# Kernel tuning notes

Measured on AMD Instinct MI355X. Metric: run time of the kernel, lower is better.

Reference implementation:

```python
import jax, jax.numpy as jnp
import numpy as np


def gcn_conv(x, W, b, src, dst):
    """PyG-style GCNConv: add self-loops, symmetric normalization, then scatter-add."""
    n = x.shape[0]
    loop = jnp.arange(n, dtype=src.dtype)
    s = jnp.concatenate([src, loop])  # [E+N]
    d = jnp.concatenate([dst, loop])
    deg = jax.ops.segment_sum(jnp.ones(s.shape[0], dtype=x.dtype), d, num_segments=n)
    dinv = jax.lax.rsqrt(jnp.maximum(deg, 1.0))  # deg >= 1 due to self-loops
    norm = dinv[s] * dinv[d]                     # [E+N]
    h = x @ W                                    # [N, out]
    msg = h[s] * norm[:, None]                   # gather + scale
    return jax.ops.segment_sum(msg, d, num_segments=n) + b


def setup_inputs() -> dict:
    key = jax.random.key(0)
    ks = jax.random.split(key, 8)
    N, E, IN, H, C = 50000, 800000, 128, 64, 16
    x = jax.random.normal(ks[0], (N, IN), dtype=jnp.float32)
    edge_index = jax.random.randint(ks[1], (2, E), 0, N, dtype=jnp.int32)
    def glorot(k, shp):
        fan_in, fan_out = shp
        lim = (6.0 / (fan_in + fan_out)) ** 0.5
        return jax.random.uniform(k, shp, jnp.float32, -lim, lim)
    return {
        "x": x,
        "edge_index": edge_index,
        "W1": glorot(ks[2], (IN, H)), "b1": jnp.zeros((H,), jnp.float32),
        "W2": glorot(ks[3], (H, H)),  "b2": jnp.zeros((H,), jnp.float32),
        "Wm1": glorot(ks[4], (2 * H, H)), "bm1": jnp.zeros((H,), jnp.float32),
        "Wm2": glorot(ks[5], (H, C)),     "bm2": jnp.zeros((C,), jnp.float32),
    }


def reference(x, edge_index, W1, b1, W2, b2, Wm1, bm1, Wm2, bm2):
    src, dst = edge_index[0], edge_index[1]
    h = jax.nn.relu(gcn_conv(x, W1, b1, src, dst))
    # dropout is identity in eval mode
    h = jax.nn.relu(gcn_conv(h, W2, b2, src, dst))
    ef = jnp.concatenate([h[src], h[dst]], axis=1)  # [E, 2H]
    z = jax.nn.relu(ef @ Wm1 + bm1)
    return z @ Wm2 + bm2  # [E, numClasses]
```

## Files before the change

### kernel.cpp

```cpp
#include <hip/hip_runtime.h>
#include <hip/hip_bf16.h>

__global__ __launch_bounds__(256) void k_deg(const int* __restrict__ dst, int* __restrict__ deg, int E) {
    int e = blockIdx.x * 256 + threadIdx.x;
    if (e < E) atomicAdd(&deg[dst[e]], 1);
}

__global__ __launch_bounds__(256) void k_dinv(const int* __restrict__ deg, float* __restrict__ dinv, int N) {
    int n = blockIdx.x * 256 + threadIdx.x;
    if (n < N) dinv[n] = rsqrtf((float)(deg[n] + 1));
}

__global__ __launch_bounds__(256) void k_scan_sum(const int* __restrict__ deg, int* __restrict__ bsum, int N) {
    int n = blockIdx.x * 256 + threadIdx.x;
    int v = (n < N) ? deg[n] : 0;
#pragma unroll
    for (int o = 32; o > 0; o >>= 1) v += __shfl_down(v, o, 64);
    __shared__ int sh[4];
    if ((threadIdx.x & 63) == 0) sh[threadIdx.x >> 6] = v;
    __syncthreads();
    if (threadIdx.x == 0) bsum[blockIdx.x] = sh[0] + sh[1] + sh[2] + sh[3];
}

__global__ __launch_bounds__(256) void k_scan_off(int* __restrict__ bsum, int nb) {
    __shared__ int sh[256];
    int t = threadIdx.x;
    sh[t] = (t < nb) ? bsum[t] : 0;
    __syncthreads();
    for (int o = 1; o < 256; o <<= 1) {
        int y = (t >= o) ? sh[t - o] : 0;
        __syncthreads();
        sh[t] += y;
        __syncthreads();
    }
    if (t < nb) bsum[t] = (t == 0) ? 0 : sh[t - 1];
}

__global__ __launch_bounds__(256) void k_scan_write(const int* __restrict__ deg, const int* __restrict__ boff,
                                                    int* __restrict__ row_start, int* __restrict__ cursor, int N) {
    int n = blockIdx.x * 256 + threadIdx.x;
    int t = threadIdx.x, lane = t & 63, w = t >> 6;
    int v = (n < N) ? deg[n] : 0;
    int x = v;
#pragma unroll
    for (int o = 1; o < 64; o <<= 1) {
        int y = __shfl_up(x, o, 64);
        if (lane >= o) x += y;
    }
    __shared__ int wsum[4];
    if (lane == 63) wsum[w] = x;
    __syncthreads();
    int wo = 0;
#pragma unroll
    for (int i = 0; i < 4; ++i) wo += (i < w) ? wsum[i] : 0;
    int excl = boff[blockIdx.x] + wo + x - v;
    if (n < N) { row_start[n] = excl; cursor[n] = excl; }
    if (n == N - 1) row_start[N] = excl + v;
}

template <bool PAIR>
__global__ __launch_bounds__(256) void k_fill(const int* __restrict__ src, const int* __restrict__ dst,
                                              int* __restrict__ cursor, void* __restrict__ item, int E) {
    int e = blockIdx.x * 256 + threadIdx.x;
    if (e < E) {
        int d = dst[e];
        int pos = atomicAdd(&cursor[d], 1);
        if (PAIR) ((int2*)item)[pos] = make_int2(src[e], e);
        else      ((int*)item)[pos] = e;
    }
}

__global__ __launch_bounds__(256) void k_dvec(const int* __restrict__ rowst, int* __restrict__ dvec, int N) {
    int w = threadIdx.x >> 6, lane = threadIdx.x & 63;
    int d = blockIdx.x * 4 + w;
    if (d >= N) return;
    int beg = rowst[d], end = rowst[d + 1];
    for (int k = beg + lane; k < end; k += 64) dvec[k] = d;
}

__global__ __launch_bounds__(256) void k_tr(const float* __restrict__ in, float* __restrict__ outp, int R, int C) {
    int i = blockIdx.x * 256 + threadIdx.x;
    if (i < R * C) {
        int r = i / C, c = i % C;
        outp[(size_t)c * R + r] = in[(size_t)r * C + c];
    }
}

__global__ __launch_bounds__(256) void k_wpq(const float* __restrict__ Wm1, float* __restrict__ WPQ) {
    int i = blockIdx.x * 256 + threadIdx.x;
    if (i < 128 * 64) {
        int j = i >> 6, k = i & 63;
        WPQ[i] = (j < 64) ? Wm1[k * 64 + j] : Wm1[(64 + k) * 64 + (j - 64)];
    }
}

template <int K, bool RELU, bool BIAS, bool SCALE>
__global__ __launch_bounds__(256) void k_mm_slice(const float* __restrict__ X,
                                                  const float* __restrict__ WT,
                                                  const float* __restrict__ bias,
                                                  const float* __restrict__ dinv,
                                                  float* __restrict__ Y, int N) {
    int n = blockIdx.x * 256 + threadIdx.x;
    int j0 = blockIdx.y * 16;
    int nc = n < N ? n : N - 1;
    const float* xr = X + (size_t)nc * K;
    const float* wr = WT + (size_t)j0 * K;
    float acc[16];
#pragma unroll
    for (int j = 0; j < 16; ++j) acc[j] = BIAS ? bias[j0 + j] : 0.f;
#pragma unroll 1
    for (int k0 = 0; k0 < K; k0 += 8) {
        float ef[8];
        *(float4*)(ef)     = *(const float4*)(xr + k0);
        *(float4*)(ef + 4) = *(const float4*)(xr + k0 + 4);
        if (RELU) {
#pragma unroll
            for (int kk = 0; kk < 8; ++kk) ef[kk] = fmaxf(ef[kk], 0.f);
        }
#pragma unroll
        for (int j = 0; j < 16; ++j) {
#pragma unroll
            for (int kk = 0; kk < 8; ++kk)
                acc[j] = fmaf(ef[kk], wr[j * K + k0 + kk], acc[j]);
        }
    }
    if (n < N) {
        if (SCALE) {
            float dn = dinv[n];
#pragma unroll
            for (int j = 0; j < 16; ++j) acc[j] *= dn;
        }
        float4* yp = (float4*)(Y + (size_t)n * 64 + j0);
#pragma unroll
        for (int q = 0; q < 4; ++q) yp[q] = *(float4*)(acc + q * 4);
    }
}

__global__ __launch_bounds__(256) void k_pq_slice(const float* __restrict__ A2,
                                                  const float* __restrict__ WPQ,
                                                  const float* __restrict__ bm1,
                                                  float* __restrict__ Pb, float* __restrict__ Qb, int N) {
    int n = blockIdx.x * 256 + threadIdx.x;
    int j0g = blockIdx.y * 16;
    bool isP = j0g < 64;
    int jo = isP ? j0g : j0g - 64;
    float* Y = isP ? Pb : Qb;
    int nc = n < N ? n : N - 1;
    const float* xr = A2 + (size_t)nc * 64;
    const float* wr = WPQ + (size_t)j0g * 64;
    float acc[16];
#pragma unroll
    for (int j = 0; j < 16; ++j) acc[j] = isP ? bm1[jo + j] : 0.f;
#pragma unroll 1
    for (int k0 = 0; k0 < 64; k0 += 8) {
        float ef[8];
        *(float4*)(ef)     = *(const float4*)(xr + k0);
        *(float4*)(ef + 4) = *(const float4*)(xr + k0 + 4);
#pragma unroll
        for (int kk = 0; kk < 8; ++kk) ef[kk] = fmaxf(ef[kk], 0.f);
#pragma unroll
        for (int j = 0; j < 16; ++j)
#pragma unroll
            for (int kk = 0; kk < 8; ++kk)
                acc[j] = fmaf(ef[kk], wr[j * 64 + k0 + kk], acc[j]);
    }
    if (n < N) {
        float4* yp = (float4*)(Y + (size_t)n * 64 + jo);
#pragma unroll
        for (int q = 0; q < 4; ++q) yp[q] = *(float4*)(acc + q * 4);
    }
}

template <bool PAIR>
__global__ __launch_bounds__(256) void k_gather(const float* __restrict__ hs, const float* __restrict__ dinv,
                                                const int* __restrict__ row_start, const void* __restrict__ item,
                                                const int* __restrict__ srcArr,
                                                const float* __restrict__ bias,
                                                float* __restrict__ a, int N) {
    int w = threadIdx.x >> 6, lane = threadIdx.x & 63;
    int d = blockIdx.x * 4 + w;
    if (d >= N) return;
    int beg = row_start[d], end = row_start[d + 1];
    float dd = dinv[d];
    float acc = hs[(size_t)d * 64 + lane];
    int k = beg;
    for (; k + 8 <= end; k += 8) {
        int ss[8];
        if (PAIR) {
            const int2* it = (const int2*)item;
#pragma unroll
            for (int u = 0; u < 8; ++u) ss[u] = it[k + u].x;
        } else {
            const int* eid = (const int*)item;
            int ee[8];
#pragma unroll
            for (int u = 0; u < 8; ++u) ee[u] = eid[k + u];
#pragma unroll
            for (int u = 0; u < 8; ++u) ss[u] = srcArr[ee[u]];
        }
        float v[8];
#pragma unroll
        for (int u = 0; u < 8; ++u) v[u] = hs[(size_t)ss[u] * 64 + lane];
#pragma unroll
        for (int u = 0; u < 8; ++u) acc += v[u];
    }
    for (; k < end; ++k) {
        int s = PAIR ? ((const int2*)item)[k].x : srcArr[((const int*)item)[k]];
        acc += hs[(size_t)s * 64 + lane];
    }
    a[(size_t)d * 64 + lane] = fmaf(acc, dd, bias[lane]);
}

__global__ __launch_bounds__(256) void k_p_inplace(float* __restrict__ A2P,
                                                   const float* __restrict__ WPQ,
                                                   const float* __restrict__ bm1, int N) {
    int n = blockIdx.x * 256 + threadIdx.x;
    int nc = n < N ? n : N - 1;
    const float* xr = A2P + (size_t)nc * 64;
    float acc[64];
#pragma unroll
    for (int j = 0; j < 64; ++j) acc[j] = bm1[j];
#pragma unroll 1
    for (int k0 = 0; k0 < 64; k0 += 8) {
        float ef[8];
        *(float4*)(ef)     = *(const float4*)(xr + k0);
        *(float4*)(ef + 4) = *(const float4*)(xr + k0 + 4);
#pragma unroll
        for (int kk = 0; kk < 8; ++kk) ef[kk] = fmaxf(ef[kk], 0.f);
#pragma unroll
        for (int j = 0; j < 64; ++j)
#pragma unroll
            for (int kk = 0; kk < 8; ++kk)
                acc[j] = fmaf(ef[kk], WPQ[j * 64 + k0 + kk], acc[j]);
    }
    if (n < N) {
#pragma unroll
        for (int q = 0; q < 16; ++q)
            *(float4*)(A2P + (size_t)n * 64 + q * 4) = *(float4*)(acc + q * 4);
    }
}

__global__ __launch_bounds__(256) void k_edge_pq(const float* __restrict__ P,
                                                 const float* __restrict__ Q,
                                                 const int* __restrict__ src,
                                                 const int* __restrict__ dst,
                                                 const float* __restrict__ W2T,
                                                 const float* __restrict__ bm2,
                                                 float* __restrict__ out, int E) {
    int e = blockIdx.x * 256 + threadIdx.x;
    int ec = e < E ? e : E - 1;
    int s = src[ec], d = dst[ec];
    const float4* p4 = (const float4*)(P + (size_t)s * 64);
    const float4* q4 = (const float4*)(Q + (size_t)d * 64);
    float z[64];
#pragma unroll
    for (int c = 0; c < 16; ++c) {
        float4 a = p4[c], b = q4[c];
        z[c * 4 + 0] = fmaxf(a.x + b.x, 0.f);
        z[c * 4 + 1] = fmaxf(a.y + b.y, 0.f);
        z[c * 4 + 2] = fmaxf(a.z + b.z, 0.f);
        z[c * 4 + 3] = fmaxf(a.w + b.w, 0.f);
    }
    float o[16];
#pragma unroll
    for (int c = 0; c < 16; ++c) {
        float a = bm2[c];
#pragma unroll
        for (int j = 0; j < 64; ++j) a = fmaf(z[j], W2T[c * 64 + j], a);
        o[c] = a;
    }
    if (e < E) {
        float4* op = (float4*)(out + (size_t)e * 16);
#pragma unroll
        for (int q = 0; q < 4; ++q) op[q] = *(float4*)(o + q * 4);
    }
}

template <bool PAIR>
__global__ __launch_bounds__(256) void k_edge_csr(const float* __restrict__ P,
                                                  const float* __restrict__ Q,
                                                  const int* __restrict__ dvec,
                                                  const void* __restrict__ item,
                                                  const int* __restrict__ srcArr,
                                                  const float* __restrict__ W2T,
                                                  const float* __restrict__ bm2,
                                                  float* __restrict__ out, int E) {
    int i = blockIdx.x * 256 + threadIdx.x;
    int ic = i < E ? i : E - 1;
    int s, e;
    if (PAIR) {
        int2 pe = ((const int2*)item)[ic];
        s = pe.x; e = pe.y;
    } else {
        e = ((const int*)item)[ic];
        s = srcArr[e];
    }
    int d = dvec[ic];
    const float4* p4 = (const float4*)(P + (size_t)s * 64);
    const float4* q4 = (const float4*)(Q + (size_t)d * 64);
    float o[16];
#pragma unroll
    for (int t = 0; t < 16; ++t) o[t] = bm2[t];
#pragma unroll
    for (int c = 0; c < 16; ++c) {
        float4 a = p4[c], b = q4[c];
        float z0 = fmaxf(a.x + b.x, 0.f);
        float z1 = fmaxf(a.y + b.y, 0.f);
        float z2 = fmaxf(a.z + b.z, 0.f);
        float z3 = fmaxf(a.w + b.w, 0.f);
#pragma unroll
        for (int t = 0; t < 16; ++t) {
            o[t] = fmaf(z0, W2T[t * 64 + c * 4 + 0], o[t]);
            o[t] = fmaf(z1, W2T[t * 64 + c * 4 + 1], o[t]);
            o[t] = fmaf(z2, W2T[t * 64 + c * 4 + 2], o[t]);
            o[t] = fmaf(z3, W2T[t * 64 + c * 4 + 3], o[t]);
        }
    }
    if (i < E) {
        float4* op = (float4*)(out + (size_t)e * 16);
#pragma unroll
        for (int q = 0; q < 4; ++q) op[q] = *(float4*)(o + q * 4);
    }
}

extern "C" void kernel_launch(void* const* d_in, const int* in_sizes, int n_in,
                              void* d_out, int out_size, void* d_ws, size_t ws_size,
                              hipStream_t stream) {
    const float* x   = (const float*)d_in[0];
    const int* ei    = (const int*)d_in[1];
    const float* W1  = (const float*)d_in[2];
    const float* b1  = (const float*)d_in[3];
    const float* W2  = (const float*)d_in[4];
    const float* b2  = (const float*)d_in[5];
    const float* Wm1 = (const float*)d_in[6];
    const float* bm1 = (const float*)d_in[7];
    const float* Wm2 = (const float*)d_in[8];
    const float* bm2 = (const float*)d_in[9];
    float* out = (float*)d_out;

    const int H  = in_sizes[3];
    const int IN = in_sizes[2] / H;
    const int N  = in_sizes[0] / IN;
    const int E  = in_sizes[1] / 2;
    const int* src = ei;
    const int* dst = ei + E;

    auto al = [](size_t b) { return (b + 255) & ~(size_t)255; };
    char* ws = (char*)d_ws;

    const size_t wb     = al((size_t)IN * H * 4) + al((size_t)H * H * 4) + al((size_t)2 * H * H * 4) + al((size_t)H * 16 * 4);
    const size_t rowstB = al(((size_t)N + 1) * 4);
    const size_t nodeB  = al((size_t)N * 64 * 4);
    const size_t pairB  = al((size_t)E * 8);
    const size_t eidB   = al((size_t)E * 4);
    const size_t needA  = wb + rowstB + pairB + 3 * nodeB;
    const size_t needB  = wb + rowstB + eidB  + 3 * nodeB;

    const int tier = (needA <= ws_size) ? 0 : (needB <= ws_size) ? 1 : 2;

    float *W1T, *W2T, *WPQ, *Wm2T, *bufB, *Qbuf, *Pbuf, *dinv;
    int *deg, *rowst, *cursor, *bsum;
    void* item;
    float* bufA = (float*)d_out;
    bool slicedP = true;

    size_t off = 0;
    auto alc = [&](size_t b) { void* p = ws + off; off += al(b); return p; };

    if (tier <= 1) {
        W1T  = (float*)alc((size_t)IN * H * 4);
        W2T  = (float*)alc((size_t)H * H * 4);
        WPQ  = (float*)alc((size_t)2 * H * H * 4);
        Wm2T = (float*)alc((size_t)H * 16 * 4);
        rowst = (int*)alc(((size_t)N + 1) * 4);
        item  = alc(tier == 0 ? (size_t)E * 8 : (size_t)E * 4);
        bufB = (float*)alc((size_t)N * 64 * 4);
        Qbuf = (float*)alc((size_t)N * 64 * 4);
        Pbuf = (float*)alc((size_t)N * 64 * 4);
        char* pz = (char*)Pbuf;
        dinv   = (float*)pz;
        deg    = (int*)(pz + al((size_t)N * 4));
        cursor = (int*)(pz + 2 * al((size_t)N * 4));
        bsum   = (int*)(pz + 3 * al((size_t)N * 4));
    } else {
        dinv = (float*)alc((size_t)N * 4);
        W1T  = (float*)alc((size_t)IN * H * 4);
        W2T  = (float*)alc((size_t)H * H * 4);
        WPQ  = (float*)alc((size_t)2 * H * H * 4);
        Wm2T = (float*)alc((size_t)H * 16 * 4);
        bufB = (float*)alc((size_t)N * 64 * 4);
        Qbuf = (float*)alc((size_t)N * 64 * 4);
        float* PbufSep = (float*)alc((size_t)N * 64 * 4);
        slicedP = (off <= ws_size);
        Pbuf = slicedP ? PbufSep : bufB;
        char* qz = (char*)Qbuf;
        size_t qo = 0;
        deg    = (int*)(qz + qo); qo += al((size_t)N * 4);
        rowst  = (int*)(qz + qo); qo += al(((size_t)N + 1) * 4);
        cursor = (int*)(qz + qo); qo += al((size_t)N * 4);
        bsum   = (int*)(qz + qo); qo += al(1024);
        item   = (void*)(qz + qo);
    }

    const int NBn = (N + 255) / 256;
    const int NBe = (E + 255) / 256;
    const int NG  = (N + 3) / 4;

    hipMemsetAsync(deg, 0, (size_t)N * sizeof(int), stream);
    k_deg<<<NBe, 256, 0, stream>>>(dst, deg, E);
    k_dinv<<<NBn, 256, 0, stream>>>(deg, dinv, N);
    k_scan_sum<<<NBn, 256, 0, stream>>>(deg, bsum, N);
    k_scan_off<<<1, 256, 0, stream>>>(bsum, NBn);
    k_scan_write<<<NBn, 256, 0, stream>>>(deg, bsum, rowst, cursor, N);
    if (tier == 1) k_fill<false><<<NBe, 256, 0, stream>>>(src, dst, cursor, item, E);
    else           k_fill<true ><<<NBe, 256, 0, stream>>>(src, dst, cursor, item, E);

    k_tr<<<(IN * H + 255) / 256, 256, 0, stream>>>(W1, W1T, IN, H);
    k_tr<<<(H * H + 255) / 256, 256, 0, stream>>>(W2, W2T, H, H);
    k_tr<<<(H * 16 + 255) / 256, 256, 0, stream>>>(Wm2, Wm2T, H, 16);
    k_wpq<<<(2 * H * H + 255) / 256, 256, 0, stream>>>(Wm1, WPQ);

    const dim3 G4(NBn, 4);
    const dim3 G8(NBn, 8);

    k_mm_slice<128, false, false, true><<<G4, 256, 0, stream>>>(x, W1T, nullptr, dinv, bufA, N);
    if (tier == 1) k_gather<false><<<NG, 256, 0, stream>>>(bufA, dinv, rowst, item, src, b1, bufB, N);
    else           k_gather<true ><<<NG, 256, 0, stream>>>(bufA, dinv, rowst, item, src, b1, bufB, N);

    k_mm_slice<64, true, false, true><<<G4, 256, 0, stream>>>(bufB, W2T, nullptr, dinv, bufA, N);
    if (tier == 1) k_gather<false><<<NG, 256, 0, stream>>>(bufA, dinv, rowst, item, src, b2, bufB, N);
    else           k_gather<true ><<<NG, 256, 0, stream>>>(bufA, dinv, rowst, item, src, b2, bufB, N);

    if (tier <= 1) {
        k_pq_slice<<<G8, 256, 0, stream>>>(bufB, WPQ, bm1, Pbuf, Qbuf, N);
        int* dvec = (int*)bufB;
        k_dvec<<<NG, 256, 0, stream>>>(rowst, dvec, N);
        if (tier == 0) k_edge_csr<true ><<<NBe, 256, 0, stream>>>(Pbuf, Qbuf, dvec, item, src, Wm2T, bm2, out, E);
        else           k_edge_csr<false><<<NBe, 256, 0, stream>>>(Pbuf, Qbuf, dvec, item, src, Wm2T, bm2, out, E);
    } else {
        k_mm_slice<64, true, false, false><<<G4, 256, 0, stream>>>(bufB, WPQ + 64 * 64, nullptr, nullptr, Qbuf, N);
        if (slicedP) k_mm_slice<64, true, true, false><<<G4, 256, 0, stream>>>(bufB, WPQ, bm1, nullptr, Pbuf, N);
        else         k_p_inplace<<<NBn, 256, 0, stream>>>(bufB, WPQ, bm1, N);
        k_edge_pq<<<NBe, 256, 0, stream>>>(Pbuf, Qbuf, src, dst, Wm2T, bm2, out, E);
    }
}
```

Measured before the change: 424.6 us.

## Fuse prep kernels, deepen gather unroll, process two edges per thread

Folds the dinv computation into the scan-sum kernel and merges the four weight-transpose/reorder kernels into a single prep kernel, cutting launch count. Adds a 16-wide unrolled loop to the CSR gather to put more loads in flight. Replaces the per-edge MLP kernel with one where each thread handles two adjacent edges, sharing the W2T weight loads and vectorizing the item/dvec reads. The two-edge variant raises register pressure and halves the thread count, which may lower occupancy.

```diff
diff --git a/kernel.cpp b/kernel.cpp
--- a/kernel.cpp
+++ b/kernel.cpp
@@ -6,18 +6,16 @@
     if (e < E) atomicAdd(&deg[dst[e]], 1);
 }
 
-__global__ __launch_bounds__(256) void k_dinv(const int* __restrict__ deg, float* __restrict__ dinv, int N) {
-    int n = blockIdx.x * 256 + threadIdx.x;
-    if (n < N) dinv[n] = rsqrtf((float)(deg[n] + 1));
-}
-
-__global__ __launch_bounds__(256) void k_scan_sum(const int* __restrict__ deg, int* __restrict__ bsum, int N) {
+__global__ __launch_bounds__(256) void k_scan_sum(const int* __restrict__ deg, int* __restrict__ bsum,
+                                                  float* __restrict__ dinv, int N) {
     int n = blockIdx.x * 256 + threadIdx.x;
     int v = (n < N) ? deg[n] : 0;
-#pragma unroll
-    for (int o = 32; o > 0; o >>= 1) v += __shfl_down(v, o, 64);
+    if (n < N) dinv[n] = rsqrtf((float)(v + 1));
+    int r = v;
+#pragma unroll
+    for (int o = 32; o > 0; o >>= 1) r += __shfl_down(r, o, 64);
     __shared__ int sh[4];
-    if ((threadIdx.x & 63) == 0) sh[threadIdx.x >> 6] = v;
+    if ((threadIdx.x & 63) == 0) sh[threadIdx.x >> 6] = r;
     __syncthreads();
     if (threadIdx.x == 0) bsum[blockIdx.x] = sh[0] + sh[1] + sh[2] + sh[3];
 }
@@ -78,17 +76,23 @@
     for (int k = beg + lane; k < end; k += 64) dvec[k] = d;
 }
 
-__global__ __launch_bounds__(256) void k_tr(const float* __restrict__ in, float* __restrict__ outp, int R, int C) {
+__global__ __launch_bounds__(256) void k_prep(const float* __restrict__ W1, const float* __restrict__ W2,
+                                              const float* __restrict__ Wm2, const float* __restrict__ Wm1,
+                                              float* __restrict__ W1T, float* __restrict__ W2T,
+                                              float* __restrict__ Wm2T, float* __restrict__ WPQ,
+                                              int IN, int H) {
     int i = blockIdx.x * 256 + threadIdx.x;
-    if (i < R * C) {
-        int r = i / C, c = i % C;
-        outp[(size_t)c * R + r] = in[(size_t)r * C + c];
-    }
-}
-
-__global__ __launch_bounds__(256) void k_wpq(const float* __restrict__ Wm1, float* __restrict__ WPQ) {
-    int i = blockIdx.x * 256 + threadIdx.x;
-    if (i < 128 * 64) {
+    int n1 = IN * H, n2 = H * H, n3 = H * 16, n4 = 2 * H * H;
+    if (i < n1) {
+        int r = i / H, c = i % H;
+        W1T[(size_t)c * IN + r] = W1[(size_t)r * H + c];
+    } else if ((i -= n1) < n2) {
+        int r = i / H, c = i % H;
+        W2T[(size_t)c * H + r] = W2[(size_t)r * H + c];
+    } else if ((i -= n2) < n3) {
+        int r = i / 16, c = i % 16;
+        Wm2T[(size_t)c * H + r] = Wm2[(size_t)r * 16 + c];
+    } else if ((i -= n3) < n4) {
         int j = i >> 6, k = i & 63;
         WPQ[i] = (j < 64) ? Wm1[k * 64 + j] : Wm1[(64 + k) * 64 + (j - 64)];
     }
@@ -184,6 +188,26 @@
     float dd = dinv[d];
     float acc = hs[(size_t)d * 64 + lane];
     int k = beg;
+    for (; k + 16 <= end; k += 16) {
+        int ss[16];
+        if (PAIR) {
+            const int2* it = (const int2*)item;
+#pragma unroll
+            for (int u = 0; u < 16; ++u) ss[u] = it[k + u].x;
+        } else {
+            const int* eid = (const int*)item;
+            int ee[16];
+#pragma unroll
+            for (int u = 0; u < 16; ++u) ee[u] = eid[k + u];
+#pragma unroll
+            for (int u = 0; u < 16; ++u) ss[u] = srcArr[ee[u]];
+        }
+        float v[16];
+#pragma unroll
+        for (int u = 0; u < 16; ++u) v[u] = hs[(size_t)ss[u] * 64 + lane];
+#pragma unroll
+        for (int u = 0; u < 16; ++u) acc += v[u];
+    }
     for (; k + 8 <= end; k += 8) {
         int ss[8];
         if (PAIR) {
@@ -277,49 +301,74 @@
 }
 
 template <bool PAIR>
-__global__ __launch_bounds__(256) void k_edge_csr(const float* __restrict__ P,
-                                                  const float* __restrict__ Q,
-                                                  const int* __restrict__ dvec,
-                                                  const void* __restrict__ item,
-                                                  const int* __restrict__ srcArr,
-                                                  const float* __restrict__ W2T,
-                                                  const float* __restrict__ bm2,
-                                                  float* __restrict__ out, int E) {
-    int i = blockIdx.x * 256 + threadIdx.x;
-    int ic = i < E ? i : E - 1;
-    int s, e;
+__global__ __launch_bounds__(256) void k_edge_csr2(const float* __restrict__ P,
+                                                   const float* __restrict__ Q,
+                                                   const int* __restrict__ dvec,
+                                                   const void* __restrict__ item,
+                                                   const int* __restrict__ srcArr,
+                                                   const float* __restrict__ W2T,
+                                                   const float* __restrict__ bm2,
+                                                   float* __restrict__ out, int E) {
+    int i0 = (blockIdx.x * 256 + threadIdx.x) * 2;
+    if (i0 >= E) return;
+    int i1 = i0 + 1;
+    bool has2 = i1 < E;
+    int s0, e0, s1, e1;
     if (PAIR) {
-        int2 pe = ((const int2*)item)[ic];
-        s = pe.x; e = pe.y;
+        if (has2) {
+            int4 pe = ((const int4*)item)[i0 >> 1];
+            s0 = pe.x; e0 = pe.y; s1 = pe.z; e1 = pe.w;
+        } else {
+            int2 pe = ((const int2*)item)[i0];
+            s0 = pe.x; e0 = pe.y; s1 = s0; e1 = e0;
+        }
     } else {
-        e = ((const int*)item)[ic];
-        s = srcArr[e];
-    }
-    int d = dvec[ic];
-    const float4* p4 = (const float4*)(P + (size_t)s * 64);
-    const float4* q4 = (const float4*)(Q + (size_t)d * 64);
-    float o[16];
-#pragma unroll
-    for (int t = 0; t < 16; ++t) o[t] = bm2[t];
-#pragma unroll
-    for (int c = 0; c < 16; ++c) {
-        float4 a = p4[c], b = q4[c];
-        float z0 = fmaxf(a.x + b.x, 0.f);
-        float z1 = fmaxf(a.y + b.y, 0.f);
-        float z2 = fmaxf(a.z + b.z, 0.f);
-        float z3 = fmaxf(a.w + b.w, 0.f);
-#pragma unroll
-        for (int t = 0; t < 16; ++t) {
-            o[t] = fmaf(z0, W2T[t * 64 + c * 4 + 0], o[t]);
-            o[t] = fmaf(z1, W2T[t * 64 + c * 4 + 1], o[t]);
-            o[t] = fmaf(z2, W2T[t * 64 + c * 4 + 2], o[t]);
-            o[t] = fmaf(z3, W2T[t * 64 + c * 4 + 3], o[t]);
-        }
-    }
-    if (i < E) {
-        float4* op = (float4*)(out + (size_t)e * 16);
-#pragma unroll
-        for (int q = 0; q < 4; ++q) op[q] = *(float4*)(o + q * 4);
+        const int* eid = (const int*)item;
+        e0 = eid[i0];
+        e1 = has2 ? eid[i1] : e0;
+        s0 = srcArr[e0];
+        s1 = srcArr[e1];
+    }
+    int d0, d1;
+    if (has2) { int2 dd = ((const int2*)dvec)[i0 >> 1]; d0 = dd.x; d1 = dd.y; }
+    else      { d0 = dvec[i0]; d1 = d0; }
+
+    const float4* p40 = (const float4*)(P + (size_t)s0 * 64);
+    const float4* p41 = (const float4*)(P + (size_t)s1 * 64);
+    const float4* q40 = (const float4*)(Q + (size_t)d0 * 64);
+    const float4* q41 = (const float4*)(Q + (size_t)d1 * 64);
+    float o0[16], o1[16];
+#pragma unroll
+    for (int u = 0; u < 16; ++u) { float b = bm2[u]; o0[u] = b; o1[u] = b; }
+#pragma unroll
+    for (int cc = 0; cc < 16; ++cc) {
+        float4 a0 = p40[cc], b0 = q40[cc];
+        float4 a1 = p41[cc], b1 = q41[cc];
+        float z00 = fmaxf(a0.x + b0.x, 0.f), z01 = fmaxf(a0.y + b0.y, 0.f);
+        float z02 = fmaxf(a0.z + b0.z, 0.f), z03 = fmaxf(a0.w + b0.w, 0.f);
+        float z10 = fmaxf(a1.x + b1.x, 0.f), z11 = fmaxf(a1.y + b1.y, 0.f);
+        float z12 = fmaxf(a1.z + b1.z, 0.f), z13 = fmaxf(a1.w + b1.w, 0.f);
+#pragma unroll
+        for (int u = 0; u < 16; ++u) {
+            float w0 = W2T[u * 64 + cc * 4 + 0];
+            float w1 = W2T[u * 64 + cc * 4 + 1];
+            float w2 = W2T[u * 64 + cc * 4 + 2];
+            float w3 = W2T[u * 64 + cc * 4 + 3];
+            o0[u] = fmaf(z00, w0, o0[u]); o1[u] = fmaf(z10, w0, o1[u]);
+            o0[u] = fmaf(z01, w1, o0[u]); o1[u] = fmaf(z11, w1, o1[u]);
+            o0[u] = fmaf(z02, w2, o0[u]); o1[u] = fmaf(z12, w2, o1[u]);
+            o0[u] = fmaf(z03, w3, o0[u]); o1[u] = fmaf(z13, w3, o1[u]);
+        }
+    }
+    {
+        float4* op = (float4*)(out + (size_t)e0 * 16);
+#pragma unroll
+        for (int q = 0; q < 4; ++q) op[q] = *(float4*)(o0 + q * 4);
+    }
+    if (has2) {
+        float4* op = (float4*)(out + (size_t)e1 * 16);
+#pragma unroll
+        for (int q = 0; q < 4; ++q) op[q] = *(float4*)(o1 + q * 4);
     }
 }
 
@@ -405,20 +454,18 @@
     const int NBn = (N + 255) / 256;
     const int NBe = (E + 255) / 256;
     const int NG  = (N + 3) / 4;
+    const int NE2 = ((E + 1) / 2 + 255) / 256;
 
     hipMemsetAsync(deg, 0, (size_t)N * sizeof(int), stream);
     k_deg<<<NBe, 256, 0, stream>>>(dst, deg, E);
-    k_dinv<<<NBn, 256, 0, stream>>>(deg, dinv, N);
-    k_scan_sum<<<NBn, 256, 0, stream>>>(deg, bsum, N);
+    k_scan_sum<<<NBn, 256, 0, stream>>>(deg, bsum, dinv, N);
     k_scan_off<<<1, 256, 0, stream>>>(bsum, NBn);
     k_scan_write<<<NBn, 256, 0, stream>>>(deg, bsum, rowst, cursor, N);
     if (tier == 1) k_fill<false><<<NBe, 256, 0, stream>>>(src, dst, cursor, item, E);
     else           k_fill<true ><<<NBe, 256, 0, stream>>>(src, dst, cursor, item, E);
 
-    k_tr<<<(IN * H + 255) / 256, 256, 0, stream>>>(W1, W1T, IN, H);
-    k_tr<<<(H * H + 255) / 256, 256, 0, stream>>>(W2, W2T, H, H);
-    k_tr<<<(H * 16 + 255) / 256, 256, 0, stream>>>(Wm2, Wm2T, H, 16);
-    k_wpq<<<(2 * H * H + 255) / 256, 256, 0, stream>>>(Wm1, WPQ);
+    const int prepElems = IN * H + H * H + H * 16 + 2 * H * H;
+    k_prep<<<(prepElems + 255) / 256, 256, 0, stream>>>(W1, W2, Wm2, Wm1, W1T, W2T, Wm2T, WPQ, IN, H);
 
     const dim3 G4(NBn, 4);
     const dim3 G8(NBn, 8);
@@ -435,8 +482,8 @@
         k_pq_slice<<<G8, 256, 0, stream>>>(bufB, WPQ, bm1, Pbuf, Qbuf, N);
         int* dvec = (int*)bufB;
         k_dvec<<<NG, 256, 0, stream>>>(rowst, dvec, N);
-        if (tier == 0) k_edge_csr<true ><<<NBe, 256, 0, stream>>>(Pbuf, Qbuf, dvec, item, src, Wm2T, bm2, out, E);
-        else           k_edge_csr<false><<<NBe, 256, 0, stream>>>(Pbuf, Qbuf, dvec, item, src, Wm2T, bm2, out, E);
+        if (tier == 0) k_edge_csr2<true ><<<NE2, 256, 0, stream>>>(Pbuf, Qbuf, dvec, item, src, Wm2T, bm2, out, E);
+        else           k_edge_csr2<false><<<NE2, 256, 0, stream>>>(Pbuf, Qbuf, dvec, item, src, Wm2T, bm2, out, E);
     } else {
         k_mm_slice<64, true, false, false><<<G4, 256, 0, stream>>>(bufB, WPQ + 64 * 64, nullptr, nullptr, Qbuf, N);
         if (slicedP) k_mm_slice<64, true, true, false><<<G4, 256, 0, stream>>>(bufB, WPQ, bm1, nullptr, Pbuf, N);
```

Result: slower. 448.8 us (+5.7%).
